# Optimization experiments

Hardware: AMD Instinct MI355X
Metric: run time of the kernel (lower is better)

## Reference

```python
import jax, jax.numpy as jnp
import numpy as np

K = 3  # deformable kernel size -> K*K = 9 sampling points
EPS = 1e-5


def _bilinear_sample(img, py, px):
    """Bilinear sample img (B,H,W,C) at float pixel coords py,px (B,H,W), zero padding."""
    B, H, W, C = img.shape
    y0f = jnp.floor(py); x0f = jnp.floor(px)
    wy = py - y0f; wx = px - x0f
    y0 = y0f.astype(jnp.int32); x0 = x0f.astype(jnp.int32)
    bidx = jnp.arange(B)[:, None, None]
    out = jnp.zeros(img.shape, img.dtype)
    corners = ((0, 0, (1 - wy) * (1 - wx)), (0, 1, (1 - wy) * wx),
               (1, 0, wy * (1 - wx)), (1, 1, wy * wx))
    for dy, dx, w in corners:
        yy = y0 + dy; xx = x0 + dx
        valid = ((yy >= 0) & (yy < H) & (xx >= 0) & (xx < W)).astype(img.dtype)
        yc = jnp.clip(yy, 0, H - 1); xc = jnp.clip(xx, 0, W - 1)
        out = out + (w * valid)[..., None] * img[bidx, yc, xc]
    return out


def setup_inputs() -> dict:
    key = jax.random.key(0)
    ks = jax.random.split(key, 8)
    B, C, H, W = 8, 256, 64, 64
    return {
        "x1": jax.random.normal(ks[0], (B, C, H, W), jnp.float32),
        "x2": jax.random.normal(ks[1], (B, C, H // 2, W // 2), jnp.float32),
        "dw_w": jax.random.normal(ks[2], (3, 3, 1, C), jnp.float32) * 0.05,
        "dw_b": jnp.zeros((C,), jnp.float32),
        "ln_g": jnp.ones((C,), jnp.float32),
        "ln_b": jnp.zeros((C,), jnp.float32),
        "off_w": jax.random.normal(ks[3], (C, 2 * K * K), jnp.float32) * 0.01,
        "off_b": jnp.zeros((2 * K * K,), jnp.float32),
        "mask_w": jax.random.normal(ks[4], (C, K * K), jnp.float32) * 0.02,
        "mask_b": jnp.zeros((K * K,), jnp.float32),
        "in_w": jax.random.normal(ks[5], (C, C), jnp.float32) * 0.02,
        "in_b": jnp.zeros((C,), jnp.float32),
        "out_w": jax.random.normal(ks[6], (C, C), jnp.float32) * 0.02,
        "out_b": jnp.zeros((C,), jnp.float32),
        "bn_g": jnp.ones((C,), jnp.float32),
        "bn_b": jnp.zeros((C,), jnp.float32),
        "bn_mean": jnp.zeros((C,), jnp.float32),
        "bn_var": jnp.ones((C,), jnp.float32),
    }


def _forward(x1, x2, dw_w, dw_b, ln_g, ln_b, off_w, off_b, mask_w, mask_b,
             in_w, in_b, out_w, out_b, bn_g, bn_b, bn_mean, bn_var):
    B, C, H, W = x1.shape
    # interpolate x2 -> (H,W), bilinear (half-pixel centers, align_corners=False)
    x2r = jax.image.resize(x2, (B, C, H, W), method="linear")
    x21, x22 = jnp.split(x2r, 2, axis=0)
    diff = jnp.abs(x21 - x22)
    guide = jnp.concatenate([diff, diff], axis=0)  # repeat(2,1,1,1)

    v = jnp.transpose(x1, (0, 2, 3, 1))      # (B,H,W,C) values
    f = jnp.transpose(guide, (0, 2, 3, 1))   # (B,H,W,C) guidance

    # DCNv3 input projection
    x_proj = v @ in_w + in_b

    # depthwise 3x3 conv + LayerNorm + GELU on guidance
    feat = jax.lax.conv_general_dilated(
        f, dw_w, (1, 1), "SAME",
        dimension_numbers=("NHWC", "HWIO", "NHWC"),
        feature_group_count=C) + dw_b
    mu = jnp.mean(feat, axis=-1, keepdims=True)
    var = jnp.var(feat, axis=-1, keepdims=True)
    feat = (feat - mu) * jax.lax.rsqrt(var + EPS) * ln_g + ln_b
    feat = jax.nn.gelu(feat)

    offset = (feat @ off_w + off_b).reshape(B, H, W, K * K, 2)  # (..., (dx,dy))
    mask = jax.nn.softmax(feat @ mask_w + mask_b, axis=-1)       # (B,H,W,9)

    base_y = jnp.arange(H, dtype=x1.dtype)[:, None]
    base_x = jnp.arange(W, dtype=x1.dtype)[None, :]
    acc = jnp.zeros((B, H, W, C), x1.dtype)
    for k in range(K * K):
        ky = k // K - 1
        kx = k % K - 1
        py = base_y + ky + offset[..., k, 1]
        px = base_x + kx + offset[..., k, 0]
        acc = acc + mask[..., k:k + 1] * _bilinear_sample(x_proj, py, px)

    y = acc @ out_w + out_b                  # output projection
    y = jnp.transpose(y, (0, 3, 1, 2))       # back to NCHW

    # BatchNorm (inference stats) + ReLU + residual
    scale = bn_g * jax.lax.rsqrt(bn_var + EPS)
    y = y * scale[None, :, None, None] + (bn_b - bn_mean * scale)[None, :, None, None]
    return jax.nn.relu(y) + x1


def reference(x1, x2, dw_w, dw_b, ln_g, ln_b, off_w, off_b, mask_w, mask_b,
              in_w, in_b, out_w, out_b, bn_g, bn_b, bn_mean, bn_var):
    return _forward(x1, x2, dw_w, dw_b, ln_g, ln_b, off_w, off_b, mask_w, mask_b,
                    in_w, in_b, out_w, out_b, bn_g, bn_b, bn_mean, bn_var)
```

## Files before the change

### kernel.cpp

```cpp
#include <hip/hip_runtime.h>
#include <math.h>

#define BB 8
#define CC 256
#define HH 64
#define WW 64
#define H2 32
#define W2 32
#define NPIX (BB*HH*WW)
#define EPSV 1e-5f

typedef unsigned short ushortT;
using short8  = __attribute__((ext_vector_type(8))) short;
using floatx4 = __attribute__((ext_vector_type(4))) float;

__device__ inline float b2f(ushortT u) {
    unsigned int x = ((unsigned int)u) << 16;
    float f; __builtin_memcpy(&f, &x, 4); return f;
}
__device__ inline ushortT f2b(float f) {
    unsigned int x; __builtin_memcpy(&x, &f, 4);
    unsigned int r = x + 0x7fffu + ((x >> 16) & 1u);
    return (ushortT)(r >> 16);
}

__global__ __launch_bounds__(256) void k0ab(const float* __restrict__ in_w,
        const float* __restrict__ in_b, const float* __restrict__ out_w,
        const float* __restrict__ off_w, const float* __restrict__ mask_w,
        ushortT* __restrict__ Bf, float* __restrict__ bwout,
        ushortT* __restrict__ Whf) {
    if (blockIdx.x >= 257) {
        int s = (blockIdx.x - 257) * 256 + threadIdx.x;
        int lane = s & 63;
        int kt = (s >> 6) & 7;
        int nt = s >> 9;
        int n = nt * 16 + (lane & 15);
        int k = kt * 32 + (lane >> 4) * 8;
        short8 o;
        #pragma unroll
        for (int j = 0; j < 8; ++j) {
            float wv = 0.f;
            int kk = k + j;
            if (n < 18)      wv = off_w[kk * 18 + n];
            else if (n < 27) wv = mask_w[kk * 9 + (n - 18)];
            o[j] = (short)f2b(wv);
        }
        *(short8*)(Whf + (size_t)s * 8) = o;
        return;
    }
    __shared__ float Wl[CC];
    int j = blockIdx.x;
    int n = threadIdx.x;
    Wl[n] = (j < CC) ? in_w[(size_t)j * CC + n] : in_b[n];
    __syncthreads();
    float acc = 0.f;
    #pragma unroll 8
    for (int k = 0; k < CC; ++k)
        acc = fmaf(Wl[k], out_w[(size_t)k * CC + n], acc);
    if (j < CC) {
        int lane = (((j >> 3) & 3) << 4) | (n & 15);
        size_t idx = ((size_t)(((n >> 4) * 8 + (j >> 5)) * 64 + lane)) * 8 + (j & 7);
        Bf[idx] = f2b(acc);
    } else {
        bwout[n] = acc;
    }
}

__global__ __launch_bounds__(256) void k1_both(const float* __restrict__ x2,
        const float* __restrict__ x1, ushortT* __restrict__ guide,
        ushortT* __restrict__ x1t) {
    __shared__ __align__(16) float Xs[2 * 64 * 2 * 33];
    __shared__ __align__(16) ushortT tile[64 * 66];
    int blk0 = blockIdx.x;
    int t = threadIdx.x;

    if (blk0 < 2048) {
        int c0 = (blk0 & 3) * 64;
        int y  = (blk0 >> 2) & 63;
        int b  = blk0 >> 8;
        int bb = b & 3;
        float sy = 0.5f * y - 0.25f;
        float fy0 = floorf(sy);
        float wy = sy - fy0;
        int jy0 = (int)fy0;
        int iy0 = max(0, min(H2 - 1, jy0));
        int iy1 = max(0, min(H2 - 1, jy0 + 1));
        #pragma unroll
        for (int i = 0; i < 8; ++i) {
            int e = t + i * 256;
            int q = e >> 10, ch = (e >> 4) & 63, r = (e >> 3) & 1, xg = (e & 7) * 4;
            int iy = r ? iy1 : iy0;
            float4 v = *(const float4*)(x2 +
                (size_t)(((bb + 4 * q) * CC + c0 + ch) * H2 + iy) * W2 + xg);
            float* dst = Xs + (size_t)((q * 64 + ch) * 2 + r) * 33 + xg;
            dst[0] = v.x; dst[1] = v.y; dst[2] = v.z; dst[3] = v.w;
        }
        __syncthreads();
        int x = t & 63, cl = t >> 6;
        float sx = 0.5f * x - 0.25f;
        float fx0 = floorf(sx);
        float wx = sx - fx0;
        int jx0 = (int)fx0;
        int ix0 = max(0, min(W2 - 1, jx0));
        int ix1 = max(0, min(W2 - 1, jx0 + 1));
        float w00 = (1.f - wy) * (1.f - wx), w01 = (1.f - wy) * wx;
        float w10 = wy * (1.f - wx), w11 = wy * wx;
        #pragma unroll
        for (int it = 0; it < 16; ++it) {
            int c = cl + it * 4;
            const float* a  = Xs + (size_t)(c * 2) * 33;
            const float* bq = Xs + (size_t)((64 + c) * 2) * 33;
            float v1 = w00 * a[ix0]  + w01 * a[ix1]  + w10 * a[33 + ix0]  + w11 * a[33 + ix1];
            float v2 = w00 * bq[ix0] + w01 * bq[ix1] + w10 * bq[33 + ix0] + w11 * bq[33 + ix1];
            tile[x * 66 + c] = f2b(fabsf(v1 - v2));
        }
        __syncthreads();
        #pragma unroll
        for (int i = 0; i < 2; ++i) {
            int e = t + i * 256;
            int px = e >> 3, oct = e & 7;
            uint4 o;
            o.x = *(const unsigned int*)(&tile[px * 66 + oct * 8 + 0]);
            o.y = *(const unsigned int*)(&tile[px * 66 + oct * 8 + 2]);
            o.z = *(const unsigned int*)(&tile[px * 66 + oct * 8 + 4]);
            o.w = *(const unsigned int*)(&tile[px * 66 + oct * 8 + 6]);
            *(uint4*)(guide + (size_t)((b * HH + y) * WW + px) * CC + c0 + oct * 8) = o;
        }
    } else {
        int blk = blk0 - 2048;
        int c0 = (blk & 3) * 64;
        int y  = (blk >> 2) & 63;
        int b  = blk >> 8;
        #pragma unroll
        for (int i = 0; i < 4; ++i) {
            int e = t + i * 256;
            int ch = e >> 4, xq = (e & 15) * 4;
            float4 v = *(const float4*)(x1 + (size_t)((b * CC + c0 + ch) * HH + y) * WW + xq);
            tile[(xq + 0) * 66 + ch] = f2b(v.x);
            tile[(xq + 1) * 66 + ch] = f2b(v.y);
            tile[(xq + 2) * 66 + ch] = f2b(v.z);
            tile[(xq + 3) * 66 + ch] = f2b(v.w);
        }
        __syncthreads();
        #pragma unroll
        for (int i = 0; i < 2; ++i) {
            int e = t + i * 256;
            int px = e >> 3, oct = e & 7;
            uint4 o;
            o.x = *(const unsigned int*)(&tile[px * 66 + oct * 8 + 0]);
            o.y = *(const unsigned int*)(&tile[px * 66 + oct * 8 + 2]);
            o.z = *(const unsigned int*)(&tile[px * 66 + oct * 8 + 4]);
            o.w = *(const unsigned int*)(&tile[px * 66 + oct * 8 + 6]);
            *(uint4*)(x1t + (size_t)((b * HH + y) * WW + px) * CC + c0 + oct * 8) = o;
        }
    }
}

__global__ __launch_bounds__(512, 4) void k2ab(const ushortT* __restrict__ guide,
        const float* __restrict__ dw_w, const float* __restrict__ dw_b,
        const float* __restrict__ ln_g, const float* __restrict__ ln_b,
        const ushortT* __restrict__ Whf, const float* __restrict__ off_b,
        const float* __restrict__ mask_b, float* __restrict__ offmask) {
    __shared__ __align__(16) short sfeat[32 * 264];
    __shared__ float O[32 * 36];
    int t = threadIdx.x;
    int blk = ((blockIdx.x & 7) << 7) | (blockIdx.x >> 3);
    int b = blk >> 7, y = (blk >> 1) & 63, xh = (blk & 1) * 32;
    int lane = t & 63, w = t >> 6;
    int cl = lane & 15, rg = lane >> 4;

    {
        int pxl = t >> 4, s = t & 15;
        int c0 = s * 16;
        int xg = xh + pxl;
        float f[16];
        #pragma unroll
        for (int q = 0; q < 4; ++q) {
            float4 d = *(const float4*)(dw_b + c0 + q * 4);
            f[q*4+0]=d.x; f[q*4+1]=d.y; f[q*4+2]=d.z; f[q*4+3]=d.w;
        }
        #pragma unroll
        for (int tap = 0; tap < 9; ++tap) {
            int dy = tap / 3 - 1, dxx = tap % 3 - 1;
            int yy = y + dy, xx = xg + dxx;
            if (yy >= 0 && yy < HH && xx >= 0 && xx < WW) {
                const ushortT* gp = guide + (size_t)((b * HH + yy) * WW + xx) * CC + c0;
                #pragma unroll
                for (int q = 0; q < 2; ++q) {
                    short8 v = *(const short8*)(gp + q * 8);
                    float4 w0 = *(const float4*)(dw_w + tap * CC + c0 + q * 8);
                    float4 w1 = *(const float4*)(dw_w + tap * CC + c0 + q * 8 + 4);
                    float wv[8] = {w0.x, w0.y, w0.z, w0.w, w1.x, w1.y, w1.z, w1.w};
                    #pragma unroll
                    for (int j2 = 0; j2 < 8; ++j2)
                        f[q*8 + j2] = fmaf(b2f((ushortT)v[j2]), wv[j2], f[q*8 + j2]);
                }
            }
        }
        float s1 = 0.f, s2 = 0.f;
        #pragma unroll
        for (int j = 0; j < 16; ++j) { s1 += f[j]; s2 += f[j] * f[j]; }
        #pragma unroll
        for (int off = 8; off; off >>= 1) {
            s1 += __shfl_xor(s1, off);
            s2 += __shfl_xor(s2, off);
        }
        float mean = s1 * (1.0f / CC);
        float var  = s2 * (1.0f / CC) - mean * mean;
        float rs = rsqrtf(var + EPSV);
        #pragma unroll
        for (int q = 0; q < 2; ++q) {
            float4 g0 = *(const float4*)(ln_g + c0 + q * 8);
            float4 g1 = *(const float4*)(ln_g + c0 + q * 8 + 4);
            float4 e0 = *(const float4*)(ln_b + c0 + q * 8);
            float4 e1 = *(const float4*)(ln_b + c0 + q * 8 + 4);
            float gv[8] = {g0.x, g0.y, g0.z, g0.w, g1.x, g1.y, g1.z, g1.w};
            float ev[8] = {e0.x, e0.y, e0.z, e0.w, e1.x, e1.y, e1.z, e1.w};
            short8 sv;
            #pragma unroll
            for (int j2 = 0; j2 < 8; ++j2) {
                float v = (f[q*8 + j2] - mean) * rs * gv[j2] + ev[j2];
                float u2 = 1.5957691216057308f * (v + 0.044715f * v * v * v);
                v = v * __frcp_rn(1.0f + __expf(-u2));
                sv[j2] = (short)f2b(v);
            }
            *(short8*)(&sfeat[pxl * 264 + c0 + q * 8]) = sv;
        }
    }
    __syncthreads();

    if (w < 4) {
        int mt = w >> 1, nt = w & 1;
        floatx4 acc = {0.f, 0.f, 0.f, 0.f};
        #pragma unroll
        for (int kt = 0; kt < 8; ++kt) {
            short8 af  = *(const short8*)(&sfeat[(mt * 16 + cl) * 264 + kt * 32 + rg * 8]);
            short8 bf2 = *(const short8*)(Whf + ((size_t)((nt * 8 + kt) * 64 + lane)) * 8);
            acc = __builtin_amdgcn_mfma_f32_16x16x32_bf16(af, bf2, acc, 0, 0, 0);
        }
        int col = nt * 16 + cl;
        float bias = (col < 18) ? off_b[col] : ((col < 27) ? mask_b[col - 18] : 0.f);
        #pragma unroll
        for (int j = 0; j < 4; ++j) {
            int row = mt * 16 + rg * 4 + j;
            O[row * 36 + col] = acc[j] + bias;
        }
    }
    __syncthreads();

    if (t < 32) {
        float* row = O + t * 36 + 18;
        float mx = row[0];
        #pragma unroll
        for (int k = 1; k < 9; ++k) mx = fmaxf(mx, row[k]);
        float e9[9], ssum = 0.f;
        #pragma unroll
        for (int k = 0; k < 9; ++k) { e9[k] = __expf(row[k] - mx); ssum += e9[k]; }
        float inv = __frcp_rn(ssum);
        #pragma unroll
        for (int k = 0; k < 9; ++k) row[k] = e9[k] * inv;
    }
    __syncthreads();
    #pragma unroll
    for (int i = 0; i < 2; ++i) {
        int idx = t + i * 512;
        int p = idx >> 5, jj = idx & 31;
        offmask[((size_t)blk * 32 + p) * 32 + jj] = O[p * 36 + jj];
    }
}

__global__ __launch_bounds__(512, 4) void k45_fused(const ushortT* __restrict__ x1t,
        const float* __restrict__ offmask, const ushortT* __restrict__ Bf,
        const float* __restrict__ bwout, const float* __restrict__ out_b,
        const float* __restrict__ bn_g, const float* __restrict__ bn_b,
        const float* __restrict__ bn_mean, const float* __restrict__ bn_var,
        const float* __restrict__ x1, float* __restrict__ out) {
    __shared__ __align__(16) char smem[30976];
    short* Asb     = (short*)smem;
    float* s_w     = (float*)(smem + 9216);
    int*   s_idx   = (int*)(smem + 18432);
    float* s_scale = (float*)(smem + 27648);
    float* s_shift = (float*)(smem + 28672);
    float* s_bw    = (float*)(smem + 29696);
    float* s_sum   = (float*)(smem + 30720);
    float* Lo      = (float*)smem;

    int t = threadIdx.x;
    int bm = ((blockIdx.x & 7) << 6) | (blockIdx.x >> 3);
    int m0 = bm * 64;
    int b = bm >> 6, y = bm & 63;
    int lane = t & 63, w = t >> 6;
    int cl = lane & 15, rg = lane >> 4;

    if (t < 256) {
        float scale = bn_g[t] * rsqrtf(bn_var[t] + EPSV);
        s_scale[t] = scale;
        s_shift[t] = out_b[t] * scale + bn_b[t] - bn_mean[t] * scale;
        s_bw[t]    = bwout[t] * scale;
    }
    for (int e = t; e < 576; e += 512) {
        int px = e / 9, k = e - px * 9;
        int p = m0 + px;
        float dxo = offmask[(size_t)p * 32 + 2 * k];
        float dyo = offmask[(size_t)p * 32 + 2 * k + 1];
        float mk  = offmask[(size_t)p * 32 + 18 + k];
        float py  = (float)y  + (float)(k / 3 - 1) + dyo;
        float pxf = (float)px + (float)(k % 3 - 1) + dxo;
        float y0f = floorf(py), x0f = floorf(pxf);
        float wy = py - y0f, wx = pxf - x0f;
        int y0 = (int)y0f, x0 = (int)x0f;
        int y1 = y0 + 1, x1i = x0 + 1;
        float vy0 = (y0 >= 0 && y0 < HH) ? 1.f : 0.f;
        float vy1 = (y1 >= 0 && y1 < HH) ? 1.f : 0.f;
        float vx0 = (x0 >= 0 && x0 < WW) ? 1.f : 0.f;
        float vx1 = (x1i >= 0 && x1i < WW) ? 1.f : 0.f;
        int yc0 = max(0, min(HH - 1, y0)), yc1 = max(0, min(HH - 1, y1));
        int xc0 = max(0, min(WW - 1, x0)), xc1 = max(0, min(WW - 1, x1i));
        int base = b * HH * WW;
        int o = (px * 9 + k) * 4;
        s_idx[o + 0] = (base + yc0 * WW + xc0) * CC;
        s_idx[o + 1] = (base + yc0 * WW + xc1) * CC;
        s_idx[o + 2] = (base + yc1 * WW + xc0) * CC;
        s_idx[o + 3] = (base + yc1 * WW + xc1) * CC;
        s_w[o + 0] = mk * (1.f - wy) * (1.f - wx) * vy0 * vx0;
        s_w[o + 1] = mk * (1.f - wy) * wx * vy0 * vx1;
        s_w[o + 2] = mk * wy * (1.f - wx) * vy1 * vx0;
        s_w[o + 3] = mk * wy * wx * vy1 * vx1;
    }
    __syncthreads();
    if (t < 64) {
        float s = 0.f;
        #pragma unroll
        for (int q = 0; q < 36; ++q) s += s_w[t * 36 + q];
        s_sum[t] = s;
    }
    __syncthreads();

    floatx4 acc[4][2];
    floatx4 zero = {0.f, 0.f, 0.f, 0.f};
    #pragma unroll
    for (int i = 0; i < 4; ++i)
        #pragma unroll
        for (int j = 0; j < 2; ++j) acc[i][j] = zero;

    for (int k0 = 0; k0 < CC; k0 += 64) {
        {
            int px = t >> 3, o8 = t & 7;
            int c = k0 + o8 * 8;
            const float* wp = s_w  + px * 36;
            const int*   ip = s_idx + px * 36;
            float f[8] = {};
            #pragma unroll
            for (int q = 0; q < 36; ++q) {
                float wv = wp[q];
                short8 v = *(const short8*)(x1t + ip[q] + c);
                #pragma unroll
                for (int j = 0; j < 8; ++j)
                    f[j] = fmaf(wv, b2f((ushortT)v[j]), f[j]);
            }
            short8 sv;
            #pragma unroll
            for (int j = 0; j < 8; ++j) sv[j] = (short)f2b(f[j]);
            *(short8*)(&Asb[px * 72 + o8 * 8]) = sv;
        }
        __syncthreads();
        int kt0 = k0 >> 5;
        #pragma unroll
        for (int kk = 0; kk < 2; ++kk) {
            short8 af[4], bfr[2];
            #pragma unroll
            for (int f = 0; f < 4; ++f)
                af[f] = *(const short8*)(&Asb[(f * 16 + cl) * 72 + kk * 32 + rg * 8]);
            #pragma unroll
            for (int fc = 0; fc < 2; ++fc)
                bfr[fc] = *(const short8*)(Bf + ((size_t)((w * 2 + fc) * 8 + kt0 + kk) * 64 + lane) * 8);
            #pragma unroll
            for (int fr = 0; fr < 4; ++fr)
                #pragma unroll
                for (int fc = 0; fc < 2; ++fc)
                    acc[fr][fc] = __builtin_amdgcn_mfma_f32_16x16x32_bf16(
                        af[fr], bfr[fc], acc[fr][fc], 0, 0, 0);
        }
        __syncthreads();
    }

    #pragma unroll
    for (int ph = 0; ph < 4; ++ph) {
        if ((w >> 1) == ph) {
            #pragma unroll
            for (int fc = 0; fc < 2; ++fc) {
                int cloc = (w & 1) * 32 + fc * 16 + cl;
                #pragma unroll
                for (int fr = 0; fr < 4; ++fr) {
                    int mr = fr * 16 + rg * 4;
                    #pragma unroll
                    for (int j = 0; j < 4; ++j)
                        Lo[(mr + j) * 65 + cloc] = acc[fr][fc][j];
                }
            }
        }
        __syncthreads();
        #pragma unroll
        for (int i = 0; i < 8; ++i) {
            int e = t + i * 512;
            int xl = e & 63, cw = e >> 6;
            int co = ph * 64 + cw;
            float val = Lo[xl * 65 + cw] * s_scale[co] + s_sum[xl] * s_bw[co] + s_shift[co];
            val = fmaxf(val, 0.f);
            size_t g = (size_t)((b * CC + co) * HH + y) * WW + xl;
            out[g] = val + x1[g];
        }
        __syncthreads();
    }
}

extern "C" void kernel_launch(void* const* d_in, const int* in_sizes, int n_in,
                              void* d_out, int out_size, void* d_ws, size_t ws_size,
                              hipStream_t stream) {
    const float* x1     = (const float*)d_in[0];
    const float* x2     = (const float*)d_in[1];
    const float* dw_w   = (const float*)d_in[2];
    const float* dw_b   = (const float*)d_in[3];
    const float* ln_g   = (const float*)d_in[4];
    const float* ln_b   = (const float*)d_in[5];
    const float* off_w  = (const float*)d_in[6];
    const float* off_b  = (const float*)d_in[7];
    const float* mask_w = (const float*)d_in[8];
    const float* mask_b = (const float*)d_in[9];
    const float* in_w   = (const float*)d_in[10];
    const float* in_b   = (const float*)d_in[11];
    const float* out_w  = (const float*)d_in[12];
    const float* out_b  = (const float*)d_in[13];
    const float* bn_g   = (const float*)d_in[14];
    const float* bn_b   = (const float*)d_in[15];
    const float* bn_mean= (const float*)d_in[16];
    const float* bn_var = (const float*)d_in[17];
    float* out = (float*)d_out;

    char* wsb = (char*)d_ws;
    const size_t SZ = (size_t)NPIX * CC * 2;
    ushortT* guide   = (ushortT*)wsb;
    ushortT* x1t     = (ushortT*)(wsb + SZ);
    float*   offmask = (float*)(wsb + 2 * SZ);
    float*   bwout   = offmask + (size_t)NPIX * 32;
    ushortT* Bf      = (ushortT*)(bwout + CC);
    ushortT* Whf     = Bf + (size_t)CC * CC;

    hipLaunchKernelGGL(k0ab,    dim3(261),  dim3(256), 0, stream, in_w, in_b, out_w,
                       off_w, mask_w, Bf, bwout, Whf);
    hipLaunchKernelGGL(k1_both, dim3(4096), dim3(256), 0, stream, x2, x1, guide, x1t);
    hipLaunchKernelGGL(k2ab,    dim3(1024), dim3(512), 0, stream, guide, dw_w, dw_b,
                       ln_g, ln_b, Whf, off_b, mask_b, offmask);
    hipLaunchKernelGGL(k45_fused, dim3(512), dim3(512), 0, stream, x1t, offmask, Bf,
                       bwout, out_b, bn_g, bn_b, bn_mean, bn_var, x1, out);
}
```

Baseline: 101.7 us.

## Double threads per block in fused deformable-gather GEMM kernel, widen K chunk

The fused gather+GEMM+epilogue kernel now runs 1024 threads per block instead of 512. Each wave owns one 16-column output tile, and the K loop steps 128 channels at a time, halving the number of gather/MFMA phases and barriers. Each gather thread still handles 8 channels of one pixel, so more threads are issuing gather loads at once. The cost is more shared memory per block, fewer accumulator registers per thread, and a launch bound of 1024 threads that may reduce the number of blocks resident per CU.

```diff
diff --git a/kernel.cpp b/kernel.cpp
--- a/kernel.cpp
+++ b/kernel.cpp
@@ -269,20 +269,20 @@
     }
 }
 
-__global__ __launch_bounds__(512, 4) void k45_fused(const ushortT* __restrict__ x1t,
+__global__ __launch_bounds__(1024, 8) void k45_fused(const ushortT* __restrict__ x1t,
         const float* __restrict__ offmask, const ushortT* __restrict__ Bf,
         const float* __restrict__ bwout, const float* __restrict__ out_b,
         const float* __restrict__ bn_g, const float* __restrict__ bn_b,
         const float* __restrict__ bn_mean, const float* __restrict__ bn_var,
         const float* __restrict__ x1, float* __restrict__ out) {
-    __shared__ __align__(16) char smem[30976];
+    __shared__ __align__(16) char smem[39168];
     short* Asb     = (short*)smem;
-    float* s_w     = (float*)(smem + 9216);
-    int*   s_idx   = (int*)(smem + 18432);
-    float* s_scale = (float*)(smem + 27648);
-    float* s_shift = (float*)(smem + 28672);
-    float* s_bw    = (float*)(smem + 29696);
-    float* s_sum   = (float*)(smem + 30720);
+    float* s_w     = (float*)(smem + 17408);
+    int*   s_idx   = (int*)(smem + 26624);
+    float* s_scale = (float*)(smem + 35840);
+    float* s_shift = (float*)(smem + 36864);
+    float* s_bw    = (float*)(smem + 37888);
+    float* s_sum   = (float*)(smem + 38912);
     float* Lo      = (float*)smem;
 
     int t = threadIdx.x;
@@ -298,7 +298,8 @@
         s_shift[t] = out_b[t] * scale + bn_b[t] - bn_mean[t] * scale;
         s_bw[t]    = bwout[t] * scale;
     }
-    for (int e = t; e < 576; e += 512) {
+    if (t < 576) {
+        int e = t;
         int px = e / 9, k = e - px * 9;
         int p = m0 + px;
         float dxo = offmask[(size_t)p * 32 + 2 * k];
@@ -336,17 +337,15 @@
     }
     __syncthreads();
 
-    floatx4 acc[4][2];
+    floatx4 acc[4];
     floatx4 zero = {0.f, 0.f, 0.f, 0.f};
     #pragma unroll
-    for (int i = 0; i < 4; ++i)
-        #pragma unroll
-        for (int j = 0; j < 2; ++j) acc[i][j] = zero;
-
-    for (int k0 = 0; k0 < CC; k0 += 64) {
+    for (int i = 0; i < 4; ++i) acc[i] = zero;
+
+    for (int k0 = 0; k0 < CC; k0 += 128) {
         {
-            int px = t >> 3, o8 = t & 7;
-            int c = k0 + o8 * 8;
+            int px = t >> 4, oct = t & 15;
+            int c = k0 + oct * 8;
             const float* wp = s_w  + px * 36;
             const int*   ip = s_idx + px * 36;
             float f[8] = {};
@@ -361,48 +360,40 @@
             short8 sv;
             #pragma unroll
             for (int j = 0; j < 8; ++j) sv[j] = (short)f2b(f[j]);
-            *(short8*)(&Asb[px * 72 + o8 * 8]) = sv;
-        }
-        __syncthreads();
-        int kt0 = k0 >> 5;
-        #pragma unroll
-        for (int kk = 0; kk < 2; ++kk) {
-            short8 af[4], bfr[2];
-            #pragma unroll
-            for (int f = 0; f < 4; ++f)
-                af[f] = *(const short8*)(&Asb[(f * 16 + cl) * 72 + kk * 32 + rg * 8]);
-            #pragma unroll
-            for (int fc = 0; fc < 2; ++fc)
-                bfr[fc] = *(const short8*)(Bf + ((size_t)((w * 2 + fc) * 8 + kt0 + kk) * 64 + lane) * 8);
+            *(short8*)(&Asb[px * 136 + oct * 8]) = sv;
+        }
+        __syncthreads();
+        int ct0 = k0 >> 5;
+        #pragma unroll
+        for (int kk = 0; kk < 4; ++kk) {
+            short8 af[4];
             #pragma unroll
             for (int fr = 0; fr < 4; ++fr)
-                #pragma unroll
-                for (int fc = 0; fc < 2; ++fc)
-                    acc[fr][fc] = __builtin_amdgcn_mfma_f32_16x16x32_bf16(
-                        af[fr], bfr[fc], acc[fr][fc], 0, 0, 0);
+                af[fr] = *(const short8*)(&Asb[(fr * 16 + cl) * 136 + kk * 32 + rg * 8]);
+            short8 bfr = *(const short8*)(Bf + ((size_t)((w * 8 + ct0 + kk) * 64 + lane)) * 8);
+            #pragma unroll
+            for (int fr = 0; fr < 4; ++fr)
+                acc[fr] = __builtin_amdgcn_mfma_f32_16x16x32_bf16(af[fr], bfr, acc[fr], 0, 0, 0);
         }
         __syncthreads();
     }
 
     #pragma unroll
     for (int ph = 0; ph < 4; ++ph) {
-        if ((w >> 1) == ph) {
-            #pragma unroll
-            for (int fc = 0; fc < 2; ++fc) {
-                int cloc = (w & 1) * 32 + fc * 16 + cl;
+        if ((w >> 2) == ph) {
+            int cloc = (w & 3) * 16 + cl;
+            #pragma unroll
+            for (int fr = 0; fr < 4; ++fr) {
+                int mr = fr * 16 + rg * 4;
                 #pragma unroll
-                for (int fr = 0; fr < 4; ++fr) {
-                    int mr = fr * 16 + rg * 4;
-                    #pragma unroll
-                    for (int j = 0; j < 4; ++j)
-                        Lo[(mr + j) * 65 + cloc] = acc[fr][fc][j];
-                }
+                for (int j = 0; j < 4; ++j)
+                    Lo[(mr + j) * 65 + cloc] = acc[fr][j];
             }
         }
         __syncthreads();
         #pragma unroll
-        for (int i = 0; i < 8; ++i) {
-            int e = t + i * 512;
+        for (int i = 0; i < 4; ++i) {
+            int e = t + i * 1024;
             int xl = e & 63, cw = e >> 6;
             int co = ph * 64 + cw;
             float val = Lo[xl * 65 + cw] * s_scale[co] + s_sum[xl] * s_bw[co] + s_shift[co];
@@ -451,6 +442,6 @@
     hipLaunchKernelGGL(k1_both, dim3(4096), dim3(256), 0, stream, x2, x1, guide, x1t);
     hipLaunchKernelGGL(k2ab,    dim3(1024), dim3(512), 0, stream, guide, dw_w, dw_b,
                        ln_g, ln_b, Whf, off_b, mask_b, offmask);
-    hipLaunchKernelGGL(k45_fused, dim3(512), dim3(512), 0, stream, x1t, offmask, Bf,
+    hipLaunchKernelGGL(k45_fused, dim3(512), dim3(1024), 0, stream, x1t, offmask, Bf,
                        bwout, out_b, bn_g, bn_b, bn_mean, bn_var, x1, out);
 }
```

Measured after the change: 148.3 us. 45.8% more time.
